# Kernel tuning notes

Measured on AMD Instinct MI355X. Metric: run time of the kernel, lower is better.

Reference implementation:

```python
import jax, jax.numpy as jnp
import numpy as np

N_NODES = 100000
N_EDGES = 3200000
D_IN = 128
D_OUT = 128


def setup_inputs() -> dict:
    key = jax.random.key(0)
    k1, k2, k3 = jax.random.split(key, 3)
    x = jax.random.normal(k1, (N_NODES, D_IN), dtype=jnp.float32)
    edge_index = jax.random.randint(k2, (2, N_EDGES), 0, N_NODES, dtype=jnp.int64)
    # Glorot-style init for the GCN linear weight [out, in]
    weight = jax.random.normal(k3, (D_OUT, D_IN), dtype=jnp.float32) * (1.0 / np.sqrt(D_IN))
    bias = jnp.zeros((D_OUT,), dtype=jnp.float32)
    return {"x": x, "edge_index": edge_index, "weight": weight, "bias": bias}


def reference(x, edge_index, weight, bias):
    """LinearEncoder.forward: (GCNConv(x, edge_index), 0).

    GCNConv: out = D^-1/2 (A + I) D^-1/2 (x W^T) + b  (symmetric norm, self-loops).
    """
    n = x.shape[0]
    src = edge_index[0]
    dst = edge_index[1]
    # add self-loops
    loops = jnp.arange(n, dtype=src.dtype)
    src = jnp.concatenate([src, loops])
    dst = jnp.concatenate([dst, loops])
    # degree (in-degree over destination nodes, unit edge weights)
    ones = jnp.ones(src.shape[0], dtype=x.dtype)
    deg = jax.ops.segment_sum(ones, dst, num_segments=n)
    deg_inv_sqrt = jnp.where(deg > 0, jax.lax.rsqrt(deg), 0.0).astype(x.dtype)
    norm = deg_inv_sqrt[src] * deg_inv_sqrt[dst]  # [E+N]
    # dense transform first (as in PyG GCNConv), then sparse aggregation
    h = x @ weight.T  # [N, D_OUT]
    msgs = h[src] * norm[:, None]  # [E+N, D_OUT]
    out = jax.ops.segment_sum(msgs, dst, num_segments=n) + bias
    return (out, 0)
```

## Files before the change

kernel.cpp:

```cpp
#include <hip/hip_runtime.h>
#include <hip/hip_bf16.h>

#define N_NODES 100000
#define N_EDGES 3200000
#define D 128

typedef unsigned short u16;

#define BKT_W 400
#define NBKT 250
#define NSH 8
#define CAPS 1856
#define CAPB (NSH * CAPS)
#define EPB 5120
#define P1B 625
#define EPT 20
#define GEMM_B 1563

typedef __attribute__((ext_vector_type(8))) short bf16x8;
typedef __attribute__((ext_vector_type(4))) float f32x4;

__device__ __forceinline__ float bf2f(u16 u) {
    union { unsigned i; float f; } a; a.i = ((unsigned)u) << 16; return a.f;
}
__device__ __forceinline__ float asf(unsigned u) {
    union { unsigned i; float f; } a; a.i = u; return a.f;
}
__device__ __forceinline__ u16 f2bf(float f) {
    __hip_bfloat16 b = __float2bfloat16(f);
    return *(u16*)&b;
}

__global__ __launch_bounds__(256) void wconv(const float* __restrict__ w,
                                             u16* __restrict__ wbf) {
    int idx = blockIdx.x * 256 + threadIdx.x;
    const float4* wp = (const float4*)(w + (size_t)idx * 8);
    float4 a = wp[0], bb = wp[1];
    union { u16 h[8]; uint4 v; } o;
    o.h[0] = f2bf(a.x); o.h[1] = f2bf(a.y);
    o.h[2] = f2bf(a.z); o.h[3] = f2bf(a.w);
    o.h[4] = f2bf(bb.x); o.h[5] = f2bf(bb.y);
    o.h[6] = f2bf(bb.z); o.h[7] = f2bf(bb.w);
    ((uint4*)wbf)[idx] = o.v;
}

__global__ __launch_bounds__(256) void p1_gemm(const int* __restrict__ ei,
                                               int* __restrict__ bcnt,
                                               unsigned* __restrict__ bbuf,
                                               const float* __restrict__ x,
                                               const u16* __restrict__ wbf,
                                               u16* __restrict__ h) {
    __shared__ unsigned s1[EPB];
    __shared__ unsigned s2[EPB];
    __shared__ int hist[NBKT], lbase[NBKT], cur[NBKT], gbase[NBKT];
    __shared__ int wsum4[4], wbase4[4];
    int t = threadIdx.x, blk = blockIdx.x;

    if (blk >= P1B) {
        int wave = t >> 6, lane = t & 63;
        int n0 = (blk - P1B) * 64 + wave * 16;
        int lrow = lane & 15;
        int quad = lane >> 4;

        int arow = n0 + lrow;
        const float* ap = x + (size_t)(arow < N_NODES ? arow : 0) * D;
        bf16x8 afrag[4];
#pragma unroll
        for (int kt = 0; kt < 4; ++kt) {
            int k0 = kt * 32 + quad * 8;
            f32x4 x0 = *(const f32x4*)(ap + k0);
            f32x4 x1 = *(const f32x4*)(ap + k0 + 4);
            bf16x8 a;
            a[0] = (short)f2bf(x0.x); a[1] = (short)f2bf(x0.y);
            a[2] = (short)f2bf(x0.z); a[3] = (short)f2bf(x0.w);
            a[4] = (short)f2bf(x1.x); a[5] = (short)f2bf(x1.y);
            a[6] = (short)f2bf(x1.z); a[7] = (short)f2bf(x1.w);
            afrag[kt] = a;
        }

#pragma unroll
        for (int jt = 0; jt < 8; ++jt) {
            int j0 = jt * 16;
            f32x4 acc = {0.f, 0.f, 0.f, 0.f};
#pragma unroll
            for (int kt = 0; kt < 4; ++kt) {
                int k0 = kt * 32 + quad * 8;
                bf16x8 b = *(const bf16x8*)(wbf + (size_t)(j0 + lrow) * D + k0);
                acc = __builtin_amdgcn_mfma_f32_16x16x32_bf16(afrag[kt], b, acc, 0, 0, 0);
            }
#pragma unroll
            for (int i = 0; i < 4; ++i) {
                int n = n0 + quad * 4 + i;
                if (n < N_NODES) h[(size_t)n * D + j0 + lrow] = f2bf(acc[i]);
            }
        }
        return;
    }

    int sh = blk & (NSH - 1);
    int e0 = blk * EPB;
    if (t < NBKT) hist[t] = 0;
    __syncthreads();

    unsigned char bk[EPT];
#pragma unroll
    for (int k = 0; k < 5; ++k) {
        int base = k * 1024 + t * 4;
        int4 s4 = *(const int4*)(ei + e0 + base);
        int4 d4 = *(const int4*)(ei + N_EDGES + e0 + base);
        int ss[4] = {s4.x, s4.y, s4.z, s4.w};
        int dd[4] = {d4.x, d4.y, d4.z, d4.w};
#pragma unroll
        for (int j = 0; j < 4; ++j) {
            unsigned bkt = (unsigned)dd[j] / BKT_W;
            unsigned dl = (unsigned)dd[j] - bkt * BKT_W;
            bk[k * 4 + j] = (unsigned char)bkt;
            s1[base + j] = ((unsigned)ss[j] << 9) | dl;
            atomicAdd(&hist[bkt], 1);
        }
    }
    __syncthreads();

    if (t < NBKT) gbase[t] = atomicAdd(&bcnt[t * NSH + sh], hist[t]);

    int lane = t & 63, wv = t >> 6;
    int hv = (t < NBKT) ? hist[t] : 0;
    int pre = hv;
#pragma unroll
    for (int o = 1; o < 64; o <<= 1) {
        int u = __shfl_up(pre, o);
        if (lane >= o) pre += u;
    }
    if (lane == 63) wsum4[wv] = pre;
    __syncthreads();
    if (t == 0) {
        int b = 0;
#pragma unroll
        for (int k = 0; k < 4; ++k) { wbase4[k] = b; b += wsum4[k]; }
    }
    __syncthreads();
    if (t < NBKT) { int ex = wbase4[wv] + pre - hv; lbase[t] = ex; cur[t] = ex; }
    __syncthreads();

#pragma unroll
    for (int k = 0; k < 5; ++k) {
        int base = k * 1024 + t * 4;
#pragma unroll
        for (int j = 0; j < 4; ++j) {
            int p = atomicAdd(&cur[bk[k * 4 + j]], 1);
            s2[p] = s1[base + j];
        }
    }
    __syncthreads();

    for (int bkt = wv; bkt < NBKT; bkt += 4) {
        int n = hist[bkt], lb = lbase[bkt], gb = gbase[bkt];
        unsigned* dst = bbuf + ((size_t)bkt * NSH + sh) * CAPS;
        for (int j = lane; j < n; j += 64) {
            int p = gb + j;
            if (p < CAPS) dst[p] = s2[lb + j];
        }
    }
}

__global__ __launch_bounds__(1024) void p2_localsort(unsigned* __restrict__ bbuf,
                                                     const int* __restrict__ bcnt,
                                                     int* __restrict__ beg_g,
                                                     int* __restrict__ cnt_g,
                                                     float* __restrict__ dinv_g) {
    __shared__ unsigned stage[CAPB];
    __shared__ int hist[BKT_W], cur[BKT_W], shcnt[NSH];
    __shared__ int wsum[8], wbase[8];
    int b = blockIdx.x, t = threadIdx.x;

    if (t < NSH) { int m = bcnt[b * NSH + t]; shcnt[t] = m > CAPS ? CAPS : m; }
    if (t < BKT_W) hist[t] = 0;
    __syncthreads();

    for (int sh = 0; sh < NSH; ++sh) {
        int m = shcnt[sh];
        const unsigned* p = bbuf + ((size_t)b * NSH + sh) * CAPS;
        for (int i = t; i < m; i += 1024) {
            unsigned w = p[i];
            stage[sh * CAPS + i] = w;
            atomicAdd(&hist[w & 511u], 1);
        }
    }
    __syncthreads();

    int lane = t & 63, wv = t >> 6;
    int hv = (t < BKT_W) ? hist[t] : 0;
    int pre = hv;
#pragma unroll
    for (int o = 1; o < 64; o <<= 1) {
        int u = __shfl_up(pre, o);
        if (lane >= o) pre += u;
    }
    if (wv < 8 && lane == 63) wsum[wv] = pre;
    __syncthreads();
    if (wv == 0) {
        int v = (lane < 8) ? wsum[lane] : 0;
        int pp = v;
#pragma unroll
        for (int o = 1; o < 8; o <<= 1) {
            int u = __shfl_up(pp, o);
            if (lane >= o) pp += u;
        }
        if (lane < 8) wbase[lane] = pp - v;
    }
    __syncthreads();
    int ex = 0;
    if (t < BKT_W) { ex = wbase[wv] + pre - hv; cur[t] = ex; }

    if (t < BKT_W) {
        int node = b * BKT_W + t;
        cnt_g[node] = hv;
        beg_g[node] = b * CAPB + ex;
        dinv_g[node] = rsqrtf((float)(hv + 1));
    }
    __syncthreads();

    int* dst = (int*)(bbuf + (size_t)b * CAPB);
    for (int sh = 0; sh < NSH; ++sh) {
        int m = shcnt[sh];
        for (int i = t; i < m; i += 1024) {
            unsigned ww = stage[sh * CAPS + i];
            int pp = atomicAdd(&cur[ww & 511u], 1);
            dst[pp] = (int)(ww >> 9);
        }
    }
}

__global__ __launch_bounds__(256) void aggregate_h2(const u16* __restrict__ h,
                                                    const float* __restrict__ dinv,
                                                    const int* __restrict__ beg_g,
                                                    const int* __restrict__ cnt_g,
                                                    const int* __restrict__ sorted_src,
                                                    const float* __restrict__ bias,
                                                    float* __restrict__ out) {
    int w = threadIdx.x >> 6;
    int l = threadIdx.x & 63;
    int n = blockIdx.x * 4 + w;
    const unsigned* h32 = (const unsigned*)h;

    float dn = dinv[n];
    unsigned us = h32[(size_t)n * 64 + l];
    float acc0 = dn * asf(us << 16);
    float acc1 = dn * asf(us & 0xffff0000u);

    int c = __builtin_amdgcn_readfirstlane(cnt_g[n]);
    int beg = __builtin_amdgcn_readfirstlane(beg_g[n]);
    const int* sp = sorted_src + beg;

    int i = 0;
    for (; i + 16 <= c; i += 16) {
        int s[16];
#pragma unroll
        for (int j = 0; j < 16; ++j) s[j] = sp[i + j];
        float dv[16];
#pragma unroll
        for (int j = 0; j < 16; ++j) dv[j] = dinv[s[j]];
        unsigned u[16];
#pragma unroll
        for (int j = 0; j < 16; ++j) u[j] = h32[(size_t)s[j] * 64 + l];
#pragma unroll
        for (int j = 0; j < 16; ++j) {
            acc0 += dv[j] * asf(u[j] << 16);
            acc1 += dv[j] * asf(u[j] & 0xffff0000u);
        }
    }
    for (; i + 4 <= c; i += 4) {
        int s0 = sp[i], s1 = sp[i + 1], s2 = sp[i + 2], s3 = sp[i + 3];
        float d0 = dinv[s0], d1 = dinv[s1], d2 = dinv[s2], d3 = dinv[s3];
        unsigned u0 = h32[(size_t)s0 * 64 + l];
        unsigned u1 = h32[(size_t)s1 * 64 + l];
        unsigned u2 = h32[(size_t)s2 * 64 + l];
        unsigned u3 = h32[(size_t)s3 * 64 + l];
        acc0 += d0 * asf(u0 << 16); acc1 += d0 * asf(u0 & 0xffff0000u);
        acc0 += d1 * asf(u1 << 16); acc1 += d1 * asf(u1 & 0xffff0000u);
        acc0 += d2 * asf(u2 << 16); acc1 += d2 * asf(u2 & 0xffff0000u);
        acc0 += d3 * asf(u3 << 16); acc1 += d3 * asf(u3 & 0xffff0000u);
    }
    for (; i < c; ++i) {
        int s = sp[i];
        float dv = dinv[s];
        unsigned u = h32[(size_t)s * 64 + l];
        acc0 += dv * asf(u << 16); acc1 += dv * asf(u & 0xffff0000u);
    }

    float2 bs = ((const float2*)bias)[l];
    float2 o;
    o.x = acc0 * dn + bs.x;
    o.y = acc1 * dn + bs.y;
    ((float2*)out)[(size_t)n * 64 + l] = o;

    if (blockIdx.x == 0 && threadIdx.x == 0) out[(size_t)N_NODES * D] = 0.f;
}

extern "C" void kernel_launch(void* const* d_in, const int* in_sizes, int n_in,
                              void* d_out, int out_size, void* d_ws, size_t ws_size,
                              hipStream_t stream) {
    const float* x = (const float*)d_in[0];
    const int* ei = (const int*)d_in[1];
    const float* w = (const float*)d_in[2];
    const float* bias = (const float*)d_in[3];
    float* out = (float*)d_out;

    char* ws = (char*)d_ws;
    size_t o = 0;
    auto alloc = [&](size_t bytes) -> char* {
        char* p = ws + o;
        o = (o + bytes + 511) & ~(size_t)511;
        return p;
    };
    u16* h = (u16*)alloc((size_t)N_NODES * D * 2);
    unsigned* bbuf = (unsigned*)alloc((size_t)NBKT * CAPB * 4);
    int* sorted = (int*)bbuf;
    int* cnt = (int*)alloc((size_t)N_NODES * 4);
    int* beg = (int*)alloc((size_t)N_NODES * 4);
    float* dinv = (float*)alloc((size_t)N_NODES * 4);
    int* bcnt = (int*)alloc((size_t)NBKT * NSH * 4);
    u16* wbf = (u16*)alloc((size_t)D * D * 2);

    hipMemsetAsync(bcnt, 0, (size_t)NBKT * NSH * 4, stream);

    wconv<<<8, 256, 0, stream>>>(w, wbf);
    p1_gemm<<<P1B + GEMM_B, 256, 0, stream>>>(ei, bcnt, bbuf, x, wbf, h);
    p2_localsort<<<NBKT, 1024, 0, stream>>>(bbuf, bcnt, beg, cnt, dinv);
    aggregate_h2<<<N_NODES / 4, 256, 0, stream>>>(h, dinv, beg, cnt, sorted, bias, out);
}
```

Before: 290.6 us.

## Fuse local sort into aggregation kernel using shared-memory source lists

Halves the bucket width to 200 nodes (500 buckets) and splits the second pass into a degree/prefix kernel plus a fused aggregation kernel. The fused kernel scatters each bucket's sources into shared memory and has waves pull nodes dynamically from an atomic counter, so the sorted edge list is never written back to or re-read from global memory. In exchange, only 500 blocks of 1024 threads run the aggregation, which may limit occupancy and load balance. Bucket edges are also read twice (once for degrees, once for the scatter).

```diff
diff --git a/kernel.cpp b/kernel.cpp
--- a/kernel.cpp
+++ b/kernel.cpp
@@ -7,11 +7,11 @@
 
 typedef unsigned short u16;
 
-#define BKT_W 400
-#define NBKT 250
+#define BKT_W 200
+#define NBKT 500
 #define NSH 8
-#define CAPS 1856
-#define CAPB (NSH * CAPS)
+#define CAPS 960
+#define SLW (NSH * CAPS)
 #define EPB 5120
 #define P1B 625
 #define EPT 20
@@ -20,9 +20,6 @@
 typedef __attribute__((ext_vector_type(8))) short bf16x8;
 typedef __attribute__((ext_vector_type(4))) float f32x4;
 
-__device__ __forceinline__ float bf2f(u16 u) {
-    union { unsigned i; float f; } a; a.i = ((unsigned)u) << 16; return a.f;
-}
 __device__ __forceinline__ float asf(unsigned u) {
     union { unsigned i; float f; } a; a.i = u; return a.f;
 }
@@ -99,10 +96,10 @@
 
     int sh = blk & (NSH - 1);
     int e0 = blk * EPB;
-    if (t < NBKT) hist[t] = 0;
-    __syncthreads();
-
-    unsigned char bk[EPT];
+    for (int i = t; i < NBKT; i += 256) hist[i] = 0;
+    __syncthreads();
+
+    unsigned short bk[EPT];
 #pragma unroll
     for (int k = 0; k < 5; ++k) {
         int base = k * 1024 + t * 4;
@@ -114,18 +111,20 @@
         for (int j = 0; j < 4; ++j) {
             unsigned bkt = (unsigned)dd[j] / BKT_W;
             unsigned dl = (unsigned)dd[j] - bkt * BKT_W;
-            bk[k * 4 + j] = (unsigned char)bkt;
+            bk[k * 4 + j] = (unsigned short)bkt;
             s1[base + j] = ((unsigned)ss[j] << 9) | dl;
             atomicAdd(&hist[bkt], 1);
         }
     }
     __syncthreads();
 
-    if (t < NBKT) gbase[t] = atomicAdd(&bcnt[t * NSH + sh], hist[t]);
+    for (int i = t; i < NBKT; i += 256)
+        gbase[i] = atomicAdd(&bcnt[i * NSH + sh], hist[i]);
 
     int lane = t & 63, wv = t >> 6;
-    int hv = (t < NBKT) ? hist[t] : 0;
-    int pre = hv;
+    int a0 = 0, a1 = 0, v = 0;
+    if (t < 250) { a0 = hist[2 * t]; a1 = hist[2 * t + 1]; v = a0 + a1; }
+    int pre = v;
 #pragma unroll
     for (int o = 1; o < 64; o <<= 1) {
         int u = __shfl_up(pre, o);
@@ -139,7 +138,11 @@
         for (int k = 0; k < 4; ++k) { wbase4[k] = b; b += wsum4[k]; }
     }
     __syncthreads();
-    if (t < NBKT) { int ex = wbase4[wv] + pre - hv; lbase[t] = ex; cur[t] = ex; }
+    if (t < 250) {
+        int ex = wbase4[wv] + pre - v;
+        lbase[2 * t] = ex;        cur[2 * t] = ex;
+        lbase[2 * t + 1] = ex + a0; cur[2 * t + 1] = ex + a0;
+    }
     __syncthreads();
 
 #pragma unroll
@@ -163,28 +166,25 @@
     }
 }
 
-__global__ __launch_bounds__(1024) void p2_localsort(unsigned* __restrict__ bbuf,
-                                                     const int* __restrict__ bcnt,
-                                                     int* __restrict__ beg_g,
-                                                     int* __restrict__ cnt_g,
-                                                     float* __restrict__ dinv_g) {
-    __shared__ unsigned stage[CAPB];
-    __shared__ int hist[BKT_W], cur[BKT_W], shcnt[NSH];
-    __shared__ int wsum[8], wbase[8];
+__global__ __launch_bounds__(256) void p2_deg(const unsigned* __restrict__ bbuf,
+                                              const int* __restrict__ bcnt,
+                                              int* __restrict__ cnt_g,
+                                              int* __restrict__ begl_g,
+                                              float* __restrict__ dinv_g) {
+    __shared__ int hist[BKT_W];
+    __shared__ int shcnt[NSH];
+    __shared__ int wsum4[4], wbase4[4];
     int b = blockIdx.x, t = threadIdx.x;
 
     if (t < NSH) { int m = bcnt[b * NSH + t]; shcnt[t] = m > CAPS ? CAPS : m; }
     if (t < BKT_W) hist[t] = 0;
     __syncthreads();
 
-    for (int sh = 0; sh < NSH; ++sh) {
-        int m = shcnt[sh];
-        const unsigned* p = bbuf + ((size_t)b * NSH + sh) * CAPS;
-        for (int i = t; i < m; i += 1024) {
-            unsigned w = p[i];
-            stage[sh * CAPS + i] = w;
-            atomicAdd(&hist[w & 511u], 1);
-        }
+    const unsigned* bb = bbuf + (size_t)b * SLW;
+    for (int i = t; i < SLW; i += 256) {
+        int shd = i / CAPS;
+        int off = i - shd * CAPS;
+        if (off < shcnt[shd]) atomicAdd(&hist[bb[i] & 511u], 1);
     }
     __syncthreads();
 
@@ -196,105 +196,118 @@
         int u = __shfl_up(pre, o);
         if (lane >= o) pre += u;
     }
-    if (wv < 8 && lane == 63) wsum[wv] = pre;
-    __syncthreads();
-    if (wv == 0) {
-        int v = (lane < 8) ? wsum[lane] : 0;
-        int pp = v;
-#pragma unroll
-        for (int o = 1; o < 8; o <<= 1) {
-            int u = __shfl_up(pp, o);
-            if (lane >= o) pp += u;
-        }
-        if (lane < 8) wbase[lane] = pp - v;
-    }
-    __syncthreads();
-    int ex = 0;
-    if (t < BKT_W) { ex = wbase[wv] + pre - hv; cur[t] = ex; }
-
+    if (lane == 63) wsum4[wv] = pre;
+    __syncthreads();
+    if (t == 0) {
+        int bb2 = 0;
+#pragma unroll
+        for (int k = 0; k < 4; ++k) { wbase4[k] = bb2; bb2 += wsum4[k]; }
+    }
+    __syncthreads();
     if (t < BKT_W) {
         int node = b * BKT_W + t;
         cnt_g[node] = hv;
-        beg_g[node] = b * CAPB + ex;
+        begl_g[node] = wbase4[wv] + pre - hv;
         dinv_g[node] = rsqrtf((float)(hv + 1));
     }
-    __syncthreads();
-
-    int* dst = (int*)(bbuf + (size_t)b * CAPB);
-    for (int sh = 0; sh < NSH; ++sh) {
-        int m = shcnt[sh];
-        for (int i = t; i < m; i += 1024) {
-            unsigned ww = stage[sh * CAPS + i];
-            int pp = atomicAdd(&cur[ww & 511u], 1);
-            dst[pp] = (int)(ww >> 9);
-        }
-    }
-}
-
-__global__ __launch_bounds__(256) void aggregate_h2(const u16* __restrict__ h,
-                                                    const float* __restrict__ dinv,
-                                                    const int* __restrict__ beg_g,
-                                                    const int* __restrict__ cnt_g,
-                                                    const int* __restrict__ sorted_src,
-                                                    const float* __restrict__ bias,
-                                                    float* __restrict__ out) {
-    int w = threadIdx.x >> 6;
-    int l = threadIdx.x & 63;
-    int n = blockIdx.x * 4 + w;
+}
+
+__global__ __launch_bounds__(1024) void agg_fused(const u16* __restrict__ h,
+                                                  const float* __restrict__ dinv,
+                                                  const int* __restrict__ cnt_g,
+                                                  const int* __restrict__ begl_g,
+                                                  const int* __restrict__ bcnt,
+                                                  const unsigned* __restrict__ bbuf,
+                                                  const float* __restrict__ bias,
+                                                  float* __restrict__ out) {
+    __shared__ int sl[SLW];
+    __shared__ int cur[BKT_W], begs[BKT_W];
+    __shared__ int shcnt[NSH];
+    __shared__ int nctr;
+    int b = blockIdx.x, t = threadIdx.x;
+
+    if (t < NSH) { int m = bcnt[b * NSH + t]; shcnt[t] = m > CAPS ? CAPS : m; }
+    if (t < BKT_W) { int e = begl_g[b * BKT_W + t]; cur[t] = e; begs[t] = e; }
+    if (t == 0) nctr = 0;
+    __syncthreads();
+
+    const unsigned* bb = bbuf + (size_t)b * SLW;
+    for (int i = t; i < SLW; i += 1024) {
+        int shd = i / CAPS;
+        int off = i - shd * CAPS;
+        if (off < shcnt[shd]) {
+            unsigned w = bb[i];
+            int pp = atomicAdd(&cur[w & 511u], 1);
+            sl[pp] = (int)(w >> 9);
+        }
+    }
+    __syncthreads();
+
     const unsigned* h32 = (const unsigned*)h;
-
-    float dn = dinv[n];
-    unsigned us = h32[(size_t)n * 64 + l];
-    float acc0 = dn * asf(us << 16);
-    float acc1 = dn * asf(us & 0xffff0000u);
-
-    int c = __builtin_amdgcn_readfirstlane(cnt_g[n]);
-    int beg = __builtin_amdgcn_readfirstlane(beg_g[n]);
-    const int* sp = sorted_src + beg;
-
-    int i = 0;
-    for (; i + 16 <= c; i += 16) {
-        int s[16];
-#pragma unroll
-        for (int j = 0; j < 16; ++j) s[j] = sp[i + j];
-        float dv[16];
-#pragma unroll
-        for (int j = 0; j < 16; ++j) dv[j] = dinv[s[j]];
-        unsigned u[16];
-#pragma unroll
-        for (int j = 0; j < 16; ++j) u[j] = h32[(size_t)s[j] * 64 + l];
-#pragma unroll
-        for (int j = 0; j < 16; ++j) {
-            acc0 += dv[j] * asf(u[j] << 16);
-            acc1 += dv[j] * asf(u[j] & 0xffff0000u);
-        }
-    }
-    for (; i + 4 <= c; i += 4) {
-        int s0 = sp[i], s1 = sp[i + 1], s2 = sp[i + 2], s3 = sp[i + 3];
-        float d0 = dinv[s0], d1 = dinv[s1], d2 = dinv[s2], d3 = dinv[s3];
-        unsigned u0 = h32[(size_t)s0 * 64 + l];
-        unsigned u1 = h32[(size_t)s1 * 64 + l];
-        unsigned u2 = h32[(size_t)s2 * 64 + l];
-        unsigned u3 = h32[(size_t)s3 * 64 + l];
-        acc0 += d0 * asf(u0 << 16); acc1 += d0 * asf(u0 & 0xffff0000u);
-        acc0 += d1 * asf(u1 << 16); acc1 += d1 * asf(u1 & 0xffff0000u);
-        acc0 += d2 * asf(u2 << 16); acc1 += d2 * asf(u2 & 0xffff0000u);
-        acc0 += d3 * asf(u3 << 16); acc1 += d3 * asf(u3 & 0xffff0000u);
-    }
-    for (; i < c; ++i) {
-        int s = sp[i];
-        float dv = dinv[s];
-        unsigned u = h32[(size_t)s * 64 + l];
-        acc0 += dv * asf(u << 16); acc1 += dv * asf(u & 0xffff0000u);
-    }
-
+    int l = t & 63;
     float2 bs = ((const float2*)bias)[l];
-    float2 o;
-    o.x = acc0 * dn + bs.x;
-    o.y = acc1 * dn + bs.y;
-    ((float2*)out)[(size_t)n * 64 + l] = o;
-
-    if (blockIdx.x == 0 && threadIdx.x == 0) out[(size_t)N_NODES * D] = 0.f;
+
+    while (true) {
+        int nl0 = 0;
+        if (l == 0) nl0 = atomicAdd(&nctr, 1);
+        int nl = __shfl(nl0, 0);
+        if (nl >= BKT_W) break;
+        int n = b * BKT_W + nl;
+
+        float dn = dinv[n];
+        unsigned us = h32[(size_t)n * 64 + l];
+        float acc0 = dn * asf(us << 16);
+        float acc1 = dn * asf(us & 0xffff0000u);
+
+        int cn = __builtin_amdgcn_readfirstlane(cnt_g[n]);
+        int lb = __builtin_amdgcn_readfirstlane(begs[nl]);
+
+        int i = 0;
+        for (; i + 16 <= cn; i += 16) {
+            int s[16];
+#pragma unroll
+            for (int j = 0; j < 16; ++j)
+                s[j] = __builtin_amdgcn_readfirstlane(sl[lb + i + j]);
+            float dv[16];
+#pragma unroll
+            for (int j = 0; j < 16; ++j) dv[j] = dinv[s[j]];
+            unsigned u[16];
+#pragma unroll
+            for (int j = 0; j < 16; ++j) u[j] = h32[(size_t)s[j] * 64 + l];
+#pragma unroll
+            for (int j = 0; j < 16; ++j) {
+                acc0 += dv[j] * asf(u[j] << 16);
+                acc1 += dv[j] * asf(u[j] & 0xffff0000u);
+            }
+        }
+        for (; i + 4 <= cn; i += 4) {
+            int s0 = __builtin_amdgcn_readfirstlane(sl[lb + i]);
+            int s1 = __builtin_amdgcn_readfirstlane(sl[lb + i + 1]);
+            int s2 = __builtin_amdgcn_readfirstlane(sl[lb + i + 2]);
+            int s3 = __builtin_amdgcn_readfirstlane(sl[lb + i + 3]);
+            float d0 = dinv[s0], d1 = dinv[s1], d2 = dinv[s2], d3 = dinv[s3];
+            unsigned u0 = h32[(size_t)s0 * 64 + l];
+            unsigned u1 = h32[(size_t)s1 * 64 + l];
+            unsigned u2 = h32[(size_t)s2 * 64 + l];
+            unsigned u3 = h32[(size_t)s3 * 64 + l];
+            acc0 += d0 * asf(u0 << 16); acc1 += d0 * asf(u0 & 0xffff0000u);
+            acc0 += d1 * asf(u1 << 16); acc1 += d1 * asf(u1 & 0xffff0000u);
+            acc0 += d2 * asf(u2 << 16); acc1 += d2 * asf(u2 & 0xffff0000u);
+            acc0 += d3 * asf(u3 << 16); acc1 += d3 * asf(u3 & 0xffff0000u);
+        }
+        for (; i < cn; ++i) {
+            int s = __builtin_amdgcn_readfirstlane(sl[lb + i]);
+            float dv = dinv[s];
+            unsigned u = h32[(size_t)s * 64 + l];
+            acc0 += dv * asf(u << 16); acc1 += dv * asf(u & 0xffff0000u);
+        }
+
+        float2 o;
+        o.x = acc0 * dn + bs.x;
+        o.y = acc1 * dn + bs.y;
+        ((float2*)out)[(size_t)n * 64 + l] = o;
+    }
+    if (b == 0 && t == 0) out[(size_t)N_NODES * D] = 0.f;
 }
 
 extern "C" void kernel_launch(void* const* d_in, const int* in_sizes, int n_in,
@@ -314,10 +327,9 @@
         return p;
     };
     u16* h = (u16*)alloc((size_t)N_NODES * D * 2);
-    unsigned* bbuf = (unsigned*)alloc((size_t)NBKT * CAPB * 4);
-    int* sorted = (int*)bbuf;
+    unsigned* bbuf = (unsigned*)alloc((size_t)NBKT * SLW * 4);
     int* cnt = (int*)alloc((size_t)N_NODES * 4);
-    int* beg = (int*)alloc((size_t)N_NODES * 4);
+    int* begl = (int*)alloc((size_t)N_NODES * 4);
     float* dinv = (float*)alloc((size_t)N_NODES * 4);
     int* bcnt = (int*)alloc((size_t)NBKT * NSH * 4);
     u16* wbf = (u16*)alloc((size_t)D * D * 2);
@@ -326,6 +338,6 @@
 
     wconv<<<8, 256, 0, stream>>>(w, wbf);
     p1_gemm<<<P1B + GEMM_B, 256, 0, stream>>>(ei, bcnt, bbuf, x, wbf, h);
-    p2_localsort<<<NBKT, 1024, 0, stream>>>(bbuf, bcnt, beg, cnt, dinv);
-    aggregate_h2<<<N_NODES / 4, 256, 0, stream>>>(h, dinv, beg, cnt, sorted, bias, out);
-}
+    p2_deg<<<NBKT, 256, 0, stream>>>(bbuf, bcnt, cnt, begl, dinv);
+    agg_fused<<<NBKT, 1024, 0, stream>>>(h, dinv, cnt, begl, bcnt, bbuf, bias, out);
+}
```

After: 295.5 us. No clear change (+1.7%).

## Split h into column chunks and aggregate per chunk with edge-parallel lanes

Applied to the files above, without the earlier changes.

The GEMM now writes h in a column-chunked layout of 8 chunks of 16 features, each stored contiguously per node. The aggregation kernel is reorganised so each block handles one chunk for 8 nodes, with each wave splitting a node's edges across 8 lane groups and combining them with xor shuffles. The aim is a smaller gathered working set per chunk (better L2 locality) and more edge-level parallelism per node. In exchange, edge indices and dinv are re-read once per chunk, 8x as many blocks are launched, and the output is written with narrower nontemporal stores.

```diff
diff --git a/kernel.cpp b/kernel.cpp
--- a/kernel.cpp
+++ b/kernel.cpp
@@ -17,12 +17,11 @@
 #define EPT 20
 #define GEMM_B 1563
 
+#define NCB 8
+
 typedef __attribute__((ext_vector_type(8))) short bf16x8;
 typedef __attribute__((ext_vector_type(4))) float f32x4;
 
-__device__ __forceinline__ float bf2f(u16 u) {
-    union { unsigned i; float f; } a; a.i = ((unsigned)u) << 16; return a.f;
-}
 __device__ __forceinline__ float asf(unsigned u) {
     union { unsigned i; float f; } a; a.i = u; return a.f;
 }
@@ -91,7 +90,8 @@
 #pragma unroll
             for (int i = 0; i < 4; ++i) {
                 int n = n0 + quad * 4 + i;
-                if (n < N_NODES) h[(size_t)n * D + j0 + lrow] = f2bf(acc[i]);
+                if (n < N_NODES)
+                    h[((size_t)jt * N_NODES + n) * 16 + lrow] = f2bf(acc[i]);
             }
         }
         return;
@@ -231,70 +231,74 @@
     }
 }
 
-__global__ __launch_bounds__(256) void aggregate_h2(const u16* __restrict__ h,
-                                                    const float* __restrict__ dinv,
-                                                    const int* __restrict__ beg_g,
-                                                    const int* __restrict__ cnt_g,
-                                                    const int* __restrict__ sorted_src,
-                                                    const float* __restrict__ bias,
-                                                    float* __restrict__ out) {
-    int w = threadIdx.x >> 6;
-    int l = threadIdx.x & 63;
-    int n = blockIdx.x * 4 + w;
-    const unsigned* h32 = (const unsigned*)h;
+__global__ __launch_bounds__(512) void agg_cs(const u16* __restrict__ h,
+                                              const float* __restrict__ dinv,
+                                              const int* __restrict__ beg_g,
+                                              const int* __restrict__ cnt_g,
+                                              const int* __restrict__ sorted_src,
+                                              const float* __restrict__ bias,
+                                              float* __restrict__ out) {
+    int blk = blockIdx.x;
+    int c = blk & (NCB - 1);
+    int chunk = blk >> 3;
+    int t = threadIdx.x;
+    int wv = t >> 6, lane = t & 63;
+    int g = lane >> 3;
+    int ll = lane & 7;
+    int n = chunk * 8 + wv;
+    const unsigned* hc = (const unsigned*)h + (size_t)c * N_NODES * 8;
 
     float dn = dinv[n];
-    unsigned us = h32[(size_t)n * 64 + l];
-    float acc0 = dn * asf(us << 16);
-    float acc1 = dn * asf(us & 0xffff0000u);
-
-    int c = __builtin_amdgcn_readfirstlane(cnt_g[n]);
-    int beg = __builtin_amdgcn_readfirstlane(beg_g[n]);
-    const int* sp = sorted_src + beg;
+    float acc0 = 0.f, acc1 = 0.f;
+    {
+        unsigned u = hc[(size_t)n * 8 + ll];
+        if (g == 0) { acc0 = dn * asf(u << 16); acc1 = dn * asf(u & 0xffff0000u); }
+    }
+
+    int cn = __builtin_amdgcn_readfirstlane(cnt_g[n]);
+    int lb = __builtin_amdgcn_readfirstlane(beg_g[n]);
+    const int* sp = sorted_src + lb;
 
     int i = 0;
-    for (; i + 16 <= c; i += 16) {
-        int s[16];
-#pragma unroll
-        for (int j = 0; j < 16; ++j) s[j] = sp[i + j];
-        float dv[16];
-#pragma unroll
-        for (int j = 0; j < 16; ++j) dv[j] = dinv[s[j]];
-        unsigned u[16];
-#pragma unroll
-        for (int j = 0; j < 16; ++j) u[j] = h32[(size_t)s[j] * 64 + l];
-#pragma unroll
-        for (int j = 0; j < 16; ++j) {
-            acc0 += dv[j] * asf(u[j] << 16);
-            acc1 += dv[j] * asf(u[j] & 0xffff0000u);
-        }
-    }
-    for (; i + 4 <= c; i += 4) {
-        int s0 = sp[i], s1 = sp[i + 1], s2 = sp[i + 2], s3 = sp[i + 3];
+    for (; i + 32 <= cn; i += 32) {
+        int s0 = __builtin_nontemporal_load(sp + i + g);
+        int s1 = __builtin_nontemporal_load(sp + i + 8 + g);
+        int s2 = __builtin_nontemporal_load(sp + i + 16 + g);
+        int s3 = __builtin_nontemporal_load(sp + i + 24 + g);
         float d0 = dinv[s0], d1 = dinv[s1], d2 = dinv[s2], d3 = dinv[s3];
-        unsigned u0 = h32[(size_t)s0 * 64 + l];
-        unsigned u1 = h32[(size_t)s1 * 64 + l];
-        unsigned u2 = h32[(size_t)s2 * 64 + l];
-        unsigned u3 = h32[(size_t)s3 * 64 + l];
+        unsigned u0 = hc[(size_t)s0 * 8 + ll];
+        unsigned u1 = hc[(size_t)s1 * 8 + ll];
+        unsigned u2 = hc[(size_t)s2 * 8 + ll];
+        unsigned u3 = hc[(size_t)s3 * 8 + ll];
         acc0 += d0 * asf(u0 << 16); acc1 += d0 * asf(u0 & 0xffff0000u);
         acc0 += d1 * asf(u1 << 16); acc1 += d1 * asf(u1 & 0xffff0000u);
         acc0 += d2 * asf(u2 << 16); acc1 += d2 * asf(u2 & 0xffff0000u);
         acc0 += d3 * asf(u3 << 16); acc1 += d3 * asf(u3 & 0xffff0000u);
     }
-    for (; i < c; ++i) {
-        int s = sp[i];
+    for (; i + 8 <= cn; i += 8) {
+        int s = __builtin_nontemporal_load(sp + i + g);
         float dv = dinv[s];
-        unsigned u = h32[(size_t)s * 64 + l];
+        unsigned u = hc[(size_t)s * 8 + ll];
         acc0 += dv * asf(u << 16); acc1 += dv * asf(u & 0xffff0000u);
     }
-
-    float2 bs = ((const float2*)bias)[l];
-    float2 o;
-    o.x = acc0 * dn + bs.x;
-    o.y = acc1 * dn + bs.y;
-    ((float2*)out)[(size_t)n * 64 + l] = o;
-
-    if (blockIdx.x == 0 && threadIdx.x == 0) out[(size_t)N_NODES * D] = 0.f;
+    if (i + g < cn) {
+        int s = sp[i + g];
+        float dv = dinv[s];
+        unsigned u = hc[(size_t)s * 8 + ll];
+        acc0 += dv * asf(u << 16); acc1 += dv * asf(u & 0xffff0000u);
+    }
+
+    acc0 += __shfl_xor(acc0, 8);  acc1 += __shfl_xor(acc1, 8);
+    acc0 += __shfl_xor(acc0, 16); acc1 += __shfl_xor(acc1, 16);
+    acc0 += __shfl_xor(acc0, 32); acc1 += __shfl_xor(acc1, 32);
+
+    if (g == 0) {
+        float2 bs = ((const float2*)bias)[c * 8 + ll];
+        float* op = out + (size_t)n * D + c * 16 + 2 * ll;
+        __builtin_nontemporal_store(acc0 * dn + bs.x, op);
+        __builtin_nontemporal_store(acc1 * dn + bs.y, op + 1);
+    }
+    if (blk == 0 && t == 0) out[(size_t)N_NODES * D] = 0.f;
 }
 
 extern "C" void kernel_launch(void* const* d_in, const int* in_sizes, int n_in,
@@ -327,5 +331,5 @@
     wconv<<<8, 256, 0, stream>>>(w, wbf);
     p1_gemm<<<P1B + GEMM_B, 256, 0, stream>>>(ei, bcnt, bbuf, x, wbf, h);
     p2_localsort<<<NBKT, 1024, 0, stream>>>(bbuf, bcnt, beg, cnt, dinv);
-    aggregate_h2<<<N_NODES / 4, 256, 0, stream>>>(h, dinv, beg, cnt, sorted, bias, out);
-}
+    agg_cs<<<(N_NODES / 8) * NCB, 512, 0, stream>>>(h, dinv, beg, cnt, sorted, bias, out);
+}
```

Measured after the change: 598.0 us. 2.06x slower.
